# Optimization experiments

Hardware: AMD Instinct MI355X
Metric: run time of the kernel (lower is better)

## Reference

```python
import jax, jax.numpy as jnp
import numpy as np

N_NODES = 50000
N_EDGES = 800000
F_IN = 128
HEADS = 2
C_HID = 64
N_GRAPHS = 32
NEG_SLOPE = 0.2
LP_LAYERS = 2
LP_ALPHA = 0.5


def gatv2_conv(x, src, dst, W_l, W_r, att, bias):
    """GATv2Conv (concat=True), edge_attr=None, self-loops already in src/dst."""
    H, C = att.shape
    N = x.shape[0]
    xl = (x @ W_l).reshape(N, H, C)  # source-side transform (x_j)
    xr = (x @ W_r).reshape(N, H, C)  # target-side transform (x_i)
    xj = xl[src]                      # [E,H,C]
    e = jax.nn.leaky_relu(xr[dst] + xj, NEG_SLOPE)
    logits = jnp.einsum('ehc,hc->eh', e, att)  # [E,H]
    # segment softmax over incoming edges of each target node
    m = jax.ops.segment_max(logits, dst, num_segments=N)
    m = jnp.where(jnp.isfinite(m), m, 0.0)
    p = jnp.exp(logits - m[dst])
    s = jax.ops.segment_sum(p, dst, num_segments=N)
    alpha = p / (s[dst] + 1e-16)
    out = jax.ops.segment_sum(xj * alpha[:, :, None], dst, num_segments=N)
    return out.reshape(N, H * C) + bias


def label_prop(y, src, dst):
    """PyG LabelPropagation: sym gcn_norm (no self-loops), clamp(0,1) post-step."""
    N = y.shape[0]
    ones = jnp.ones(src.shape[0], dtype=y.dtype)
    deg = jax.ops.segment_sum(ones, dst, num_segments=N)
    dinv = jnp.where(deg > 0, jax.lax.rsqrt(jnp.maximum(deg, 1.0)), 0.0)
    w = (dinv[src] * dinv[dst])[:, None]
    res = (1.0 - LP_ALPHA) * y
    out = y
    for _ in range(LP_LAYERS):
        out = LP_ALPHA * jax.ops.segment_sum(out[src] * w, dst, num_segments=N) + res
        out = jnp.clip(out, 0.0, 1.0)
    return out


def setup_inputs() -> dict:
    key = jax.random.key(0)
    ks = jax.random.split(key, 16)
    HC = HEADS * C_HID

    def glorot(k, shape):
        lim = np.sqrt(6.0 / (shape[0] + shape[-1]))
        return jax.random.uniform(k, shape, jnp.float32, -lim, lim)

    x = jax.random.normal(ks[0], (N_NODES, F_IN), jnp.float32)
    edge_index = jax.random.randint(ks[1], (2, N_EDGES), 0, N_NODES, jnp.int32)
    batch = jnp.sort(jax.random.randint(ks[2], (N_NODES,), 0, N_GRAPHS, jnp.int32))
    return {
        'x': x, 'edge_index': edge_index, 'batch': batch,
        'W_l1': glorot(ks[3], (F_IN, HC)), 'W_r1': glorot(ks[4], (F_IN, HC)),
        'att1': glorot(ks[5], (HEADS, C_HID)), 'b1': jnp.zeros((HC,), jnp.float32),
        'W_l2': glorot(ks[6], (HC, HC)), 'W_r2': glorot(ks[7], (HC, HC)),
        'att2': glorot(ks[8], (HEADS, C_HID)), 'b2': jnp.zeros((HC,), jnp.float32),
        'mlp_W1': glorot(ks[9], (F_IN + 2 * HC, 256)), 'mlp_b1': jnp.zeros((256,), jnp.float32),
        'mlp_W2': glorot(ks[10], (256, 128)), 'mlp_b2': jnp.zeros((128,), jnp.float32),
    }


def reference(x, edge_index, batch, W_l1, W_r1, att1, b1, W_l2, W_r2, att2, b2,
              mlp_W1, mlp_b1, mlp_W2, mlp_b2):
    N = x.shape[0]
    src, dst = edge_index[0], edge_index[1]
    # GATv2Conv adds self-loops by default
    loop = jnp.arange(N, dtype=src.dtype)
    src_sl = jnp.concatenate([src, loop])
    dst_sl = jnp.concatenate([dst, loop])

    h0 = x
    h1 = jax.nn.elu(gatv2_conv(h0, src_sl, dst_sl, W_l1, W_r1, att1, b1))
    h1 = label_prop(h1, src, dst)
    h2 = jax.nn.elu(gatv2_conv(h1, src_sl, dst_sl, W_l2, W_r2, att2, b2))
    h2 = label_prop(h2, src, dst)

    combined = jnp.concatenate([h0, h1, h2], axis=-1)  # [N, 384]
    # global mean pool over graphs
    sums = jax.ops.segment_sum(combined, batch, num_segments=N_GRAPHS)
    cnts = jax.ops.segment_sum(jnp.ones((N,), combined.dtype), batch, num_segments=N_GRAPHS)
    g = sums / jnp.maximum(cnts, 1.0)[:, None]  # [G, 384]

    h = jax.nn.relu(g @ mlp_W1 + mlp_b1)  # dropout is identity in eval
    return h @ mlp_W2 + mlp_b2
```

## Files before the change

### kernel.cpp

```cpp
#include <hip/hip_runtime.h>
#include <math.h>

#define FDIM 128
#define NEG_SLOPE 0.2f
#define LP_ALPHA 0.5f
#define NGRAPHS 32
#define POOLF 384
#define MLP_H 256
#define OUT_F 128
#define POOL_CH 8

#define LRELU(z) ((z) > 0.0f ? (z) : NEG_SLOPE * (z))

__global__ void count_deg_k(const int* __restrict__ dst, int* __restrict__ deg, int E) {
    int e = blockIdx.x * blockDim.x + threadIdx.x;
    if (e < E) atomicAdd(&deg[dst[e]], 1);
}

__global__ __launch_bounds__(256) void scan_part_k(const int* __restrict__ deg,
                                                   int* __restrict__ tileSum, int N) {
    int b = blockIdx.x, t = threadIdx.x;
    int base = b * 1024 + t * 4;
    int v = 0;
    if (base + 3 < N) { int4 d = *(const int4*)(deg + base); v = d.x + d.y + d.z + d.w; }
    else if (base < N) {
        v = deg[base];
        if (base + 1 < N) v += deg[base + 1];
        if (base + 2 < N) v += deg[base + 2];
    }
#pragma unroll
    for (int off = 32; off > 0; off >>= 1) v += __shfl_xor(v, off, 64);
    __shared__ int ws[4];
    if ((t & 63) == 0) ws[t >> 6] = v;
    __syncthreads();
    if (t == 0) tileSum[b] = ws[0] + ws[1] + ws[2] + ws[3];
}

__global__ void scan_tiles_k(const int* __restrict__ tileSum, int* __restrict__ tileOff, int nt) {
    int t = threadIdx.x;
    int v = (t < nt) ? tileSum[t] : 0;
    int incl = v;
#pragma unroll
    for (int off = 1; off < 64; off <<= 1) {
        int u = __shfl_up(incl, off, 64);
        if (t >= off) incl += u;
    }
    if (t < nt) tileOff[t] = incl - v;
}

__global__ __launch_bounds__(256) void scan_write_k(const int* __restrict__ deg,
                                                    const int* __restrict__ tileOff,
                                                    int* __restrict__ row_ptr,
                                                    int* __restrict__ cursor,
                                                    float* __restrict__ dinv, int N, int E) {
    int b = blockIdx.x, t = threadIdx.x;
    int base = b * 1024 + t * 4;
    int d0 = 0, d1 = 0, d2 = 0, d3 = 0;
    if (base + 3 < N) { int4 d = *(const int4*)(deg + base); d0 = d.x; d1 = d.y; d2 = d.z; d3 = d.w; }
    else if (base < N) {
        d0 = deg[base];
        if (base + 1 < N) d1 = deg[base + 1];
        if (base + 2 < N) d2 = deg[base + 2];
    }
    int lsum = d0 + d1 + d2 + d3;
    int lane = t & 63, wv = t >> 6;
    int incl = lsum;
#pragma unroll
    for (int off = 1; off < 64; off <<= 1) {
        int u = __shfl_up(incl, off, 64);
        if (lane >= off) incl += u;
    }
    __shared__ int wsum[4];
    if (lane == 63) wsum[wv] = incl;
    __syncthreads();
    int woff = 0;
#pragma unroll
    for (int k = 0; k < 4; ++k) if (k < wv) woff += wsum[k];
    int off0 = tileOff[b] + woff + (incl - lsum);
    if (base < N)     { row_ptr[base]     = off0;                cursor[base]     = off0;
                        dinv[base]     = d0 > 0 ? 1.0f / sqrtf((float)d0) : 0.0f; }
    if (base + 1 < N) { row_ptr[base + 1] = off0 + d0;           cursor[base + 1] = off0 + d0;
                        dinv[base + 1] = d1 > 0 ? 1.0f / sqrtf((float)d1) : 0.0f; }
    if (base + 2 < N) { row_ptr[base + 2] = off0 + d0 + d1;      cursor[base + 2] = off0 + d0 + d1;
                        dinv[base + 2] = d2 > 0 ? 1.0f / sqrtf((float)d2) : 0.0f; }
    if (base + 3 < N) { row_ptr[base + 3] = off0 + d0 + d1 + d2; cursor[base + 3] = off0 + d0 + d1 + d2;
                        dinv[base + 3] = d3 > 0 ? 1.0f / sqrtf((float)d3) : 0.0f; }
    if (b == 0 && t == 0) row_ptr[N] = E;
}

__global__ void scatter_k(const int* __restrict__ src, const int* __restrict__ dst,
                          int* __restrict__ cursor, const float* __restrict__ dinv,
                          int2* __restrict__ elist, int E) {
    int e = blockIdx.x * blockDim.x + threadIdx.x;
    if (e >= E) return;
    int d = dst[e], s = src[e];
    int pos = atomicAdd(&cursor[d], 1);
    unsigned long long v = (unsigned int)s |
                           ((unsigned long long)(unsigned int)__float_as_int(dinv[s]) << 32);
    __builtin_nontemporal_store(v, (unsigned long long*)&elist[pos]);
}

__global__ void gbound_k(const int* __restrict__ batch, int* __restrict__ gb, int N) {
    int g = threadIdx.x;
    if (g > NGRAPHS) return;
    int lo = 0, hi = N;
    while (lo < hi) {
        int mid = (lo + hi) >> 1;
        if (batch[mid] < g) lo = mid + 1; else hi = mid;
    }
    gb[g] = lo;
}

__global__ __launch_bounds__(512) void gemm128x2_k(const float* __restrict__ X,
                                                   const float* __restrict__ Wl,
                                                   const float* __restrict__ Wr,
                                                   float* __restrict__ Yl,
                                                   float* __restrict__ Yr, int N) {
    __shared__ float Xs[FDIM][68];
    int t = threadIdx.x;
    int r0 = blockIdx.x * 64;
    for (int idx = t; idx < 64 * FDIM; idx += 512) {
        int k = idx & 127, r = idx >> 7;
        int row = r0 + r;
        Xs[k][r] = (row < N) ? X[(size_t)row * FDIM + k] : 0.0f;
    }
    __syncthreads();
    int tr = t >> 5;
    int tc = t & 31;
    float accl[4][4] = {{0.f}}, accr[4][4] = {{0.f}};
#pragma unroll 4
    for (int k = 0; k < FDIM; ++k) {
        float4 bl = *(const float4*)(Wl + k * FDIM + tc * 4);
        float4 br = *(const float4*)(Wr + k * FDIM + tc * 4);
        float4 a = *(const float4*)(&Xs[k][tr * 4]);
        float av[4] = {a.x, a.y, a.z, a.w};
#pragma unroll
        for (int r = 0; r < 4; ++r) {
            accl[r][0] = fmaf(av[r], bl.x, accl[r][0]);
            accl[r][1] = fmaf(av[r], bl.y, accl[r][1]);
            accl[r][2] = fmaf(av[r], bl.z, accl[r][2]);
            accl[r][3] = fmaf(av[r], bl.w, accl[r][3]);
            accr[r][0] = fmaf(av[r], br.x, accr[r][0]);
            accr[r][1] = fmaf(av[r], br.y, accr[r][1]);
            accr[r][2] = fmaf(av[r], br.z, accr[r][2]);
            accr[r][3] = fmaf(av[r], br.w, accr[r][3]);
        }
    }
#pragma unroll
    for (int r = 0; r < 4; ++r) {
        int row = r0 + tr * 4 + r;
        if (row < N) {
            *(float4*)(Yl + (size_t)row * FDIM + tc * 4) =
                make_float4(accl[r][0], accl[r][1], accl[r][2], accl[r][3]);
            *(float4*)(Yr + (size_t)row * FDIM + tc * 4) =
                make_float4(accr[r][0], accr[r][1], accr[r][2], accr[r][3]);
        }
    }
}

__global__ __launch_bounds__(256) void gat_pull_k(const float* __restrict__ xl,
                                                  const float* __restrict__ xr,
                                                  const int* __restrict__ row_ptr,
                                                  const int2* __restrict__ elist,
                                                  const float* __restrict__ att,
                                                  const float* __restrict__ bias,
                                                  float* __restrict__ out, int N) {
    int wid = threadIdx.x >> 6;
    int lane = threadIdx.x & 63;
    int qw = lane >> 4;
    int lq = lane & 15;
    int i = blockIdx.x * 4 + wid;
    if (i >= N) return;
    int cbase = 8 * lq;
    float4 at0 = *(const float4*)(att + cbase);
    float4 at1 = *(const float4*)(att + cbase + 4);
    size_t ibase = (size_t)i * FDIM + cbase;
    float4 xr0 = *(const float4*)(xr + ibase);
    float4 xr1 = *(const float4*)(xr + ibase + 4);
    float4 xs0 = *(const float4*)(xl + ibase);
    float4 xs1 = *(const float4*)(xl + ibase + 4);

    auto qdot = [&](float4 x0, float4 x1) {
        float v = LRELU(xr0.x + x0.x) * at0.x + LRELU(xr0.y + x0.y) * at0.y
                + LRELU(xr0.z + x0.z) * at0.z + LRELU(xr0.w + x0.w) * at0.w
                + LRELU(xr1.x + x1.x) * at1.x + LRELU(xr1.y + x1.y) * at1.y
                + LRELU(xr1.z + x1.z) * at1.z + LRELU(xr1.w + x1.w) * at1.w;
        v += __shfl_xor(v, 1, 64);
        v += __shfl_xor(v, 2, 64);
        v += __shfl_xor(v, 4, 64);
        return v;
    };

    const float4 z4 = make_float4(0.f, 0.f, 0.f, 0.f);
    float lself = qdot(xs0, xs1);
    bool q0 = (qw == 0);
    float mA = q0 ? lself : -INFINITY, sA = q0 ? 1.0f : 0.0f;
    float4 aA0 = q0 ? xs0 : z4, aA1 = q0 ? xs1 : z4;
    float mB = -INFINITY, sB = 0.0f;
    float4 aB0 = z4, aB1 = z4;

    int beg = row_ptr[i], end = row_ptr[i + 1];
    for (int p = beg; p < end; p += 8) {
        int i0 = p + qw, i1 = p + 4 + qw;
        bool v0 = i0 < end, v1 = i1 < end;
        int j0 = elist[min(i0, end - 1)].x;
        int j1 = elist[min(i1, end - 1)].x;
        const float* b0 = xl + (size_t)j0 * FDIM + cbase;
        const float* b1 = xl + (size_t)j1 * FDIM + cbase;
        float4 x00 = *(const float4*)(b0), x01 = *(const float4*)(b0 + 4);
        float4 x10 = *(const float4*)(b1), x11 = *(const float4*)(b1 + 4);
        float l0 = qdot(x00, x01);
        float l1 = qdot(x10, x11);
        if (v0) {
            float mn = fmaxf(mA, l0);
            float sc = __expf(mA - mn), pe = __expf(l0 - mn);
            sA = fmaf(sA, sc, pe);
            aA0.x = fmaf(aA0.x, sc, pe * x00.x); aA0.y = fmaf(aA0.y, sc, pe * x00.y);
            aA0.z = fmaf(aA0.z, sc, pe * x00.z); aA0.w = fmaf(aA0.w, sc, pe * x00.w);
            aA1.x = fmaf(aA1.x, sc, pe * x01.x); aA1.y = fmaf(aA1.y, sc, pe * x01.y);
            aA1.z = fmaf(aA1.z, sc, pe * x01.z); aA1.w = fmaf(aA1.w, sc, pe * x01.w);
            mA = mn;
        }
        if (v1) {
            float mn = fmaxf(mB, l1);
            float sc = __expf(mB - mn), pe = __expf(l1 - mn);
            sB = fmaf(sB, sc, pe);
            aB0.x = fmaf(aB0.x, sc, pe * x10.x); aB0.y = fmaf(aB0.y, sc, pe * x10.y);
            aB0.z = fmaf(aB0.z, sc, pe * x10.z); aB0.w = fmaf(aB0.w, sc, pe * x10.w);
            aB1.x = fmaf(aB1.x, sc, pe * x11.x); aB1.y = fmaf(aB1.y, sc, pe * x11.y);
            aB1.z = fmaf(aB1.z, sc, pe * x11.z); aB1.w = fmaf(aB1.w, sc, pe * x11.w);
            mB = mn;
        }
    }
    {
        float mn = fmaxf(mA, mB);
        float cA = (mA == -INFINITY) ? 0.0f : __expf(mA - mn);
        float cB = (mB == -INFINITY) ? 0.0f : __expf(mB - mn);
        sA = sA * cA + sB * cB;
        aA0.x = aA0.x * cA + aB0.x * cB; aA0.y = aA0.y * cA + aB0.y * cB;
        aA0.z = aA0.z * cA + aB0.z * cB; aA0.w = aA0.w * cA + aB0.w * cB;
        aA1.x = aA1.x * cA + aB1.x * cB; aA1.y = aA1.y * cA + aB1.y * cB;
        aA1.z = aA1.z * cA + aB1.z * cB; aA1.w = aA1.w * cA + aB1.w * cB;
        mA = mn;
    }
#pragma unroll
    for (int mask = 16; mask <= 32; mask <<= 1) {
        float pm = __shfl_xor(mA, mask, 64);
        float ps = __shfl_xor(sA, mask, 64);
        float p0x = __shfl_xor(aA0.x, mask, 64), p0y = __shfl_xor(aA0.y, mask, 64);
        float p0z = __shfl_xor(aA0.z, mask, 64), p0w = __shfl_xor(aA0.w, mask, 64);
        float p1x = __shfl_xor(aA1.x, mask, 64), p1y = __shfl_xor(aA1.y, mask, 64);
        float p1z = __shfl_xor(aA1.z, mask, 64), p1w = __shfl_xor(aA1.w, mask, 64);
        float mn = fmaxf(mA, pm);
        float cA = (mA == -INFINITY) ? 0.0f : __expf(mA - mn);
        float cP = (pm == -INFINITY) ? 0.0f : __expf(pm - mn);
        sA = sA * cA + ps * cP;
        aA0.x = aA0.x * cA + p0x * cP; aA0.y = aA0.y * cA + p0y * cP;
        aA0.z = aA0.z * cA + p0z * cP; aA0.w = aA0.w * cA + p0w * cP;
        aA1.x = aA1.x * cA + p1x * cP; aA1.y = aA1.y * cA + p1y * cP;
        aA1.z = aA1.z * cA + p1z * cP; aA1.w = aA1.w * cA + p1w * cP;
        mA = mn;
    }
    if (qw == 0) {
        float inv = 1.0f / (sA + 1e-16f);
        float4 bv0 = *(const float4*)(bias + cbase);
        float4 bv1 = *(const float4*)(bias + cbase + 4);
        float z0 = aA0.x * inv + bv0.x, z1 = aA0.y * inv + bv0.y;
        float z2 = aA0.z * inv + bv0.z, z3 = aA0.w * inv + bv0.w;
        float z4_ = aA1.x * inv + bv1.x, z5 = aA1.y * inv + bv1.y;
        float z6 = aA1.z * inv + bv1.z, z7 = aA1.w * inv + bv1.w;
        float4 o0, o1;
        o0.x = (z0 > 0.f) ? z0 : (__expf(z0) - 1.f);
        o0.y = (z1 > 0.f) ? z1 : (__expf(z1) - 1.f);
        o0.z = (z2 > 0.f) ? z2 : (__expf(z2) - 1.f);
        o0.w = (z3 > 0.f) ? z3 : (__expf(z3) - 1.f);
        o1.x = (z4_ > 0.f) ? z4_ : (__expf(z4_) - 1.f);
        o1.y = (z5 > 0.f) ? z5 : (__expf(z5) - 1.f);
        o1.z = (z6 > 0.f) ? z6 : (__expf(z6) - 1.f);
        o1.w = (z7 > 0.f) ? z7 : (__expf(z7) - 1.f);
        *(float4*)(out + ibase) = o0;
        *(float4*)(out + ibase + 4) = o1;
    }
}

__global__ __launch_bounds__(256) void lp_pull_k(const float* __restrict__ y,
                                                 const float* __restrict__ cur,
                                                 float* __restrict__ nxt,
                                                 const int* __restrict__ row_ptr,
                                                 const int2* __restrict__ elist,
                                                 const float* __restrict__ dinv, int N) {
    int wid = threadIdx.x >> 6, lane = threadIdx.x & 63;
    int half = lane >> 5, lh = lane & 31;
    int i = blockIdx.x * 4 + wid;
    if (i >= N) return;
    int beg = row_ptr[i], end = row_ptr[i + 1];
    float4 a0 = make_float4(0.f, 0.f, 0.f, 0.f), a1 = a0, a2 = a0, a3 = a0;
    for (int p = beg; p < end; p += 8) {
        int i0 = p + half, i1 = p + 2 + half, i2 = p + 4 + half, i3 = p + 6 + half;
        int2 e0 = elist[min(i0, end - 1)];
        int2 e1 = elist[min(i1, end - 1)];
        int2 e2 = elist[min(i2, end - 1)];
        int2 e3 = elist[min(i3, end - 1)];
        float w0 = (i0 < end) ? __int_as_float(e0.y) : 0.0f;
        float w1 = (i1 < end) ? __int_as_float(e1.y) : 0.0f;
        float w2 = (i2 < end) ? __int_as_float(e2.y) : 0.0f;
        float w3 = (i3 < end) ? __int_as_float(e3.y) : 0.0f;
        float4 x0 = *(const float4*)(cur + (size_t)e0.x * FDIM + 4 * lh);
        float4 x1 = *(const float4*)(cur + (size_t)e1.x * FDIM + 4 * lh);
        float4 x2 = *(const float4*)(cur + (size_t)e2.x * FDIM + 4 * lh);
        float4 x3 = *(const float4*)(cur + (size_t)e3.x * FDIM + 4 * lh);
        a0.x = fmaf(w0, x0.x, a0.x); a0.y = fmaf(w0, x0.y, a0.y);
        a0.z = fmaf(w0, x0.z, a0.z); a0.w = fmaf(w0, x0.w, a0.w);
        a1.x = fmaf(w1, x1.x, a1.x); a1.y = fmaf(w1, x1.y, a1.y);
        a1.z = fmaf(w1, x1.z, a1.z); a1.w = fmaf(w1, x1.w, a1.w);
        a2.x = fmaf(w2, x2.x, a2.x); a2.y = fmaf(w2, x2.y, a2.y);
        a2.z = fmaf(w2, x2.z, a2.z); a2.w = fmaf(w2, x2.w, a2.w);
        a3.x = fmaf(w3, x3.x, a3.x); a3.y = fmaf(w3, x3.y, a3.y);
        a3.z = fmaf(w3, x3.z, a3.z); a3.w = fmaf(w3, x3.w, a3.w);
    }
    float4 a;
    a.x = (a0.x + a1.x) + (a2.x + a3.x);
    a.y = (a0.y + a1.y) + (a2.y + a3.y);
    a.z = (a0.z + a1.z) + (a2.z + a3.z);
    a.w = (a0.w + a1.w) + (a2.w + a3.w);
    a.x += __shfl_xor(a.x, 32, 64);
    a.y += __shfl_xor(a.y, 32, 64);
    a.z += __shfl_xor(a.z, 32, 64);
    a.w += __shfl_xor(a.w, 32, 64);
    if (half == 0) {
        float di = dinv[i];
        size_t ibase = (size_t)i * FDIM + 4 * lh;
        float4 yv = *(const float4*)(y + ibase);
        float4 o;
        o.x = fminf(fmaxf(fmaf(LP_ALPHA * di, a.x, (1.0f - LP_ALPHA) * yv.x), 0.f), 1.f);
        o.y = fminf(fmaxf(fmaf(LP_ALPHA * di, a.y, (1.0f - LP_ALPHA) * yv.y), 0.f), 1.f);
        o.z = fminf(fmaxf(fmaf(LP_ALPHA * di, a.z, (1.0f - LP_ALPHA) * yv.z), 0.f), 1.f);
        o.w = fminf(fmaxf(fmaf(LP_ALPHA * di, a.w, (1.0f - LP_ALPHA) * yv.w), 0.f), 1.f);
        *(float4*)(nxt + ibase) = o;
    }
}

__global__ void pool_part_k(const float* __restrict__ x, const float* __restrict__ h1,
                            const float* __restrict__ h2, const int* __restrict__ gb,
                            float* __restrict__ part) {
    int g = blockIdx.x, si = blockIdx.y, ch = blockIdx.z;
    int t = threadIdx.x;
    const float* s = (si == 0) ? x : ((si == 1) ? h1 : h2);
    int n0g = gb[g], n1g = gb[g + 1];
    int len = n1g - n0g;
    int per = (len + POOL_CH - 1) / POOL_CH;
    int n0 = n0g + ch * per;
    int n1 = min(n0 + per, n1g);
    float acc = 0.0f;
    for (int n = n0; n < n1; ++n) acc += s[(size_t)n * FDIM + t];
    part[(((g * 3 + si) << 3) + ch) * FDIM + t] = acc;
}

__global__ void mlp1_k(const float* __restrict__ part, const int* __restrict__ gb,
                       const float* __restrict__ W1, const float* __restrict__ b1,
                       float* __restrict__ h) {
    int g = blockIdx.x;
    int t = threadIdx.x;
    __shared__ float gm[POOLF];
    int cnt = gb[g + 1] - gb[g];
    float inv = 1.0f / fmaxf((float)cnt, 1.0f);
    for (int f = t; f < POOLF; f += 256) {
        int si = f >> 7, fl = f & 127;
        float s = 0.0f;
#pragma unroll
        for (int c = 0; c < POOL_CH; ++c)
            s += part[(((g * 3 + si) << 3) + c) * FDIM + fl];
        gm[f] = s * inv;
    }
    __syncthreads();
    float acc = b1[t];
    for (int k = 0; k < POOLF; ++k) acc = fmaf(gm[k], W1[k * MLP_H + t], acc);
    h[g * MLP_H + t] = fmaxf(acc, 0.0f);
}

__global__ void mlp2_k(const float* __restrict__ h, const float* __restrict__ W2,
                       const float* __restrict__ b2, float* __restrict__ out) {
    int g = blockIdx.x;
    int t = threadIdx.x;
    __shared__ float hs[MLP_H];
    for (int k = t; k < MLP_H; k += 128) hs[k] = h[g * MLP_H + k];
    __syncthreads();
    float acc = b2[t];
    for (int k = 0; k < MLP_H; ++k) acc = fmaf(hs[k], W2[k * OUT_F + t], acc);
    out[g * OUT_F + t] = acc;
}

extern "C" void kernel_launch(void* const* d_in, const int* in_sizes, int n_in,
                              void* d_out, int out_size, void* d_ws, size_t ws_size,
                              hipStream_t stream) {
    const float* x    = (const float*)d_in[0];
    const int*   ei   = (const int*)d_in[1];
    const int*   batch= (const int*)d_in[2];
    const float* W_l1 = (const float*)d_in[3];
    const float* W_r1 = (const float*)d_in[4];
    const float* att1 = (const float*)d_in[5];
    const float* b1   = (const float*)d_in[6];
    const float* W_l2 = (const float*)d_in[7];
    const float* W_r2 = (const float*)d_in[8];
    const float* att2 = (const float*)d_in[9];
    const float* b2   = (const float*)d_in[10];
    const float* mW1  = (const float*)d_in[11];
    const float* mb1  = (const float*)d_in[12];
    const float* mW2  = (const float*)d_in[13];
    const float* mb2  = (const float*)d_in[14];
    float* out = (float*)d_out;

    const int N = in_sizes[2];
    const int E = in_sizes[1] / 2;
    const int* src = ei;
    const int* dst = ei + E;

    char* w = (char*)d_ws;
    auto alloc = [&](size_t bytes) -> char* {
        char* p = w;
        w += (bytes + 255) & ~(size_t)255;
        return p;
    };
    float* bufA = (float*)alloc((size_t)N * FDIM * 4);
    float* bufB = (float*)alloc((size_t)N * FDIM * 4);
    float* bufC = (float*)alloc((size_t)N * FDIM * 4);
    float* bufD = (float*)alloc((size_t)N * FDIM * 4);
    int* deg     = (int*)alloc((size_t)N * 4);
    int* cursor  = (int*)alloc((size_t)N * 4);
    int* row_lp  = (int*)alloc((size_t)(N + 1) * 4);
    int2* elist  = (int2*)alloc((size_t)E * 8);
    float* dinv  = (float*)alloc((size_t)N * 4);
    int* gb      = (int*)alloc((size_t)(NGRAPHS + 1) * 4);
    int* tileSum = (int*)alloc((size_t)64 * 4);
    int* tileOff = (int*)alloc((size_t)64 * 4);
    float* part  = (float*)alloc((size_t)NGRAPHS * 3 * POOL_CH * FDIM * 4);
    float* mlp_h = (float*)alloc((size_t)NGRAPHS * MLP_H * 4);

    const int TB = 256;
    int gE = (E + TB - 1) / TB;
    int nTiles = (N + 1023) / 1024;

    hipMemsetAsync(deg, 0, (size_t)N * 4, stream);
    count_deg_k<<<gE, TB, 0, stream>>>(dst, deg, E);
    gbound_k<<<1, 64, 0, stream>>>(batch, gb, N);
    scan_part_k<<<nTiles, 256, 0, stream>>>(deg, tileSum, N);
    scan_tiles_k<<<1, 64, 0, stream>>>(tileSum, tileOff, nTiles);
    scan_write_k<<<nTiles, 256, 0, stream>>>(deg, tileOff, row_lp, cursor, dinv, N, E);
    scatter_k<<<gE, TB, 0, stream>>>(src, dst, cursor, dinv, elist, E);

    int gGemm = (N + 63) / 64;
    int gWave = (N + 3) / 4;

    gemm128x2_k<<<gGemm, 512, 0, stream>>>(x, W_l1, W_r1, bufA, bufB, N);
    gat_pull_k<<<gWave, 256, 0, stream>>>(bufA, bufB, row_lp, elist, att1, b1, bufC, N);
    lp_pull_k<<<gWave, 256, 0, stream>>>(bufC, bufC, bufA, row_lp, elist, dinv, N);
    lp_pull_k<<<gWave, 256, 0, stream>>>(bufC, bufA, bufC, row_lp, elist, dinv, N);

    gemm128x2_k<<<gGemm, 512, 0, stream>>>(bufC, W_l2, W_r2, bufA, bufB, N);
    gat_pull_k<<<gWave, 256, 0, stream>>>(bufA, bufB, row_lp, elist, att2, b2, bufD, N);
    lp_pull_k<<<gWave, 256, 0, stream>>>(bufD, bufD, bufA, row_lp, elist, dinv, N);
    lp_pull_k<<<gWave, 256, 0, stream>>>(bufD, bufA, bufD, row_lp, elist, dinv, N);

    pool_part_k<<<dim3(NGRAPHS, 3, POOL_CH), 128, 0, stream>>>(x, bufC, bufD, gb, part);

    mlp1_k<<<NGRAPHS, 256, 0, stream>>>(part, gb, mW1, mb1, mlp_h);
    mlp2_k<<<NGRAPHS, 128, 0, stream>>>(mlp_h, mW2, mb2, out);
}
```

Baseline: 781.5 us.

## Tile GEMM over K with register-prefetched shared X and W chunks

The dual-output 128x128 GEMM now stages both X and the two weight matrices through shared memory in 16-wide K chunks. The next chunk is prefetched into registers while the current one is computed. Each thread now computes 8 rows instead of 4, and the block size drops from 512 to 256 threads. This removes the per-iteration global loads of W and the large whole-X LDS tile, at the cost of more registers per thread and two syncs per chunk.

```diff
diff --git a/kernel.cpp b/kernel.cpp
--- a/kernel.cpp
+++ b/kernel.cpp
@@ -9,6 +9,7 @@
 #define MLP_H 256
 #define OUT_F 128
 #define POOL_CH 8
+#define GCH 16
 
 #define LRELU(z) ((z) > 0.0f ? (z) : NEG_SLOPE * (z))
 
@@ -111,44 +112,79 @@
     gb[g] = lo;
 }
 
-__global__ __launch_bounds__(512) void gemm128x2_k(const float* __restrict__ X,
+__global__ __launch_bounds__(256) void gemm128x2_k(const float* __restrict__ X,
                                                    const float* __restrict__ Wl,
                                                    const float* __restrict__ Wr,
                                                    float* __restrict__ Yl,
                                                    float* __restrict__ Yr, int N) {
-    __shared__ float Xs[FDIM][68];
+    __shared__ float Xs[GCH][68];
+    __shared__ float Ws[2][GCH][128];
     int t = threadIdx.x;
     int r0 = blockIdx.x * 64;
-    for (int idx = t; idx < 64 * FDIM; idx += 512) {
-        int k = idx & 127, r = idx >> 7;
-        int row = r0 + r;
-        Xs[k][r] = (row < N) ? X[(size_t)row * FDIM + k] : 0.0f;
-    }
-    __syncthreads();
+
+    int xrow = t >> 2;
+    int xk4  = t & 3;
+    int xg   = r0 + xrow;
+    float4 wreg[4];
+    float4 xreg;
+
+    auto LOADC = [&](int k0) {
+        xreg = (xg < N) ? *(const float4*)(X + (size_t)xg * FDIM + k0 + xk4 * 4)
+                        : make_float4(0.f, 0.f, 0.f, 0.f);
+#pragma unroll
+        for (int j = 0; j < 4; ++j) {
+            int idx = t + 256 * j;
+            int mat = idx >> 9, kr = (idx >> 5) & 15, c4 = idx & 31;
+            const float* Wp = mat ? Wr : Wl;
+            wreg[j] = *(const float4*)(Wp + (k0 + kr) * FDIM + c4 * 4);
+        }
+    };
+    auto STOREC = [&]() {
+        Xs[xk4 * 4 + 0][xrow] = xreg.x;
+        Xs[xk4 * 4 + 1][xrow] = xreg.y;
+        Xs[xk4 * 4 + 2][xrow] = xreg.z;
+        Xs[xk4 * 4 + 3][xrow] = xreg.w;
+#pragma unroll
+        for (int j = 0; j < 4; ++j) {
+            int idx = t + 256 * j;
+            int mat = idx >> 9, kr = (idx >> 5) & 15, c4 = idx & 31;
+            *(float4*)(&Ws[mat][kr][c4 * 4]) = wreg[j];
+        }
+    };
+
     int tr = t >> 5;
     int tc = t & 31;
-    float accl[4][4] = {{0.f}}, accr[4][4] = {{0.f}};
-#pragma unroll 4
-    for (int k = 0; k < FDIM; ++k) {
-        float4 bl = *(const float4*)(Wl + k * FDIM + tc * 4);
-        float4 br = *(const float4*)(Wr + k * FDIM + tc * 4);
-        float4 a = *(const float4*)(&Xs[k][tr * 4]);
-        float av[4] = {a.x, a.y, a.z, a.w};
-#pragma unroll
-        for (int r = 0; r < 4; ++r) {
-            accl[r][0] = fmaf(av[r], bl.x, accl[r][0]);
-            accl[r][1] = fmaf(av[r], bl.y, accl[r][1]);
-            accl[r][2] = fmaf(av[r], bl.z, accl[r][2]);
-            accl[r][3] = fmaf(av[r], bl.w, accl[r][3]);
-            accr[r][0] = fmaf(av[r], br.x, accr[r][0]);
-            accr[r][1] = fmaf(av[r], br.y, accr[r][1]);
-            accr[r][2] = fmaf(av[r], br.z, accr[r][2]);
-            accr[r][3] = fmaf(av[r], br.w, accr[r][3]);
+    float accl[8][4] = {{0.f}}, accr[8][4] = {{0.f}};
+
+    LOADC(0);
+    for (int c = 0; c < FDIM / GCH; ++c) {
+        __syncthreads();
+        STOREC();
+        __syncthreads();
+        if (c + 1 < FDIM / GCH) LOADC((c + 1) * GCH);
+#pragma unroll
+        for (int kk = 0; kk < GCH; ++kk) {
+            float4 bl = *(const float4*)(&Ws[0][kk][tc * 4]);
+            float4 br = *(const float4*)(&Ws[1][kk][tc * 4]);
+            float4 a0 = *(const float4*)(&Xs[kk][tr * 8]);
+            float4 a1 = *(const float4*)(&Xs[kk][tr * 8 + 4]);
+            float av[8] = {a0.x, a0.y, a0.z, a0.w, a1.x, a1.y, a1.z, a1.w};
+#pragma unroll
+            for (int r = 0; r < 8; ++r) {
+                accl[r][0] = fmaf(av[r], bl.x, accl[r][0]);
+                accl[r][1] = fmaf(av[r], bl.y, accl[r][1]);
+                accl[r][2] = fmaf(av[r], bl.z, accl[r][2]);
+                accl[r][3] = fmaf(av[r], bl.w, accl[r][3]);
+                accr[r][0] = fmaf(av[r], br.x, accr[r][0]);
+                accr[r][1] = fmaf(av[r], br.y, accr[r][1]);
+                accr[r][2] = fmaf(av[r], br.z, accr[r][2]);
+                accr[r][3] = fmaf(av[r], br.w, accr[r][3]);
+            }
         }
     }
 #pragma unroll
-    for (int r = 0; r < 4; ++r) {
-        int row = r0 + tr * 4 + r;
+    for (int r = 0; r < 8; ++r) {
+        int row = r0 + tr * 8 + r;
         if (row < N) {
             *(float4*)(Yl + (size_t)row * FDIM + tc * 4) =
                 make_float4(accl[r][0], accl[r][1], accl[r][2], accl[r][3]);
@@ -451,12 +487,12 @@
     int gGemm = (N + 63) / 64;
     int gWave = (N + 3) / 4;
 
-    gemm128x2_k<<<gGemm, 512, 0, stream>>>(x, W_l1, W_r1, bufA, bufB, N);
+    gemm128x2_k<<<gGemm, 256, 0, stream>>>(x, W_l1, W_r1, bufA, bufB, N);
     gat_pull_k<<<gWave, 256, 0, stream>>>(bufA, bufB, row_lp, elist, att1, b1, bufC, N);
     lp_pull_k<<<gWave, 256, 0, stream>>>(bufC, bufC, bufA, row_lp, elist, dinv, N);
     lp_pull_k<<<gWave, 256, 0, stream>>>(bufC, bufA, bufC, row_lp, elist, dinv, N);
 
-    gemm128x2_k<<<gGemm, 512, 0, stream>>>(bufC, W_l2, W_r2, bufA, bufB, N);
+    gemm128x2_k<<<gGemm, 256, 0, stream>>>(bufC, W_l2, W_r2, bufA, bufB, N);
     gat_pull_k<<<gWave, 256, 0, stream>>>(bufA, bufB, row_lp, elist, att2, b2, bufD, N);
     lp_pull_k<<<gWave, 256, 0, stream>>>(bufD, bufD, bufA, row_lp, elist, dinv, N);
     lp_pull_k<<<gWave, 256, 0, stream>>>(bufD, bufA, bufD, row_lp, elist, dinv, N);
```

After: 762.3 us. 1.03x faster.
